# Performance work log

Hardware: AMD Instinct MI355X
Metric: run time of the kernel (lower is better)

The kernel has to match this reference:

```python
import jax, jax.numpy as jnp
import numpy as np

B, S, W = 32, 256, 32
T = 16               # topics per doc, each spanning L = S//T sentences
VOCAB, E, H, D = 400001, 300, 128, 128


def _gru_scan(x, Wih, Whh, bih, bhh, reverse=False):
    """x: [B,S,E] -> (outputs [B,S,H], final hidden [B,H]). Torch GRU cell math."""
    h0 = jnp.zeros((x.shape[0], Whh.shape[1]), x.dtype)
    gi_all = jnp.einsum('bse,ge->bsg', x, Wih) + bih  # precompute input gates [B,S,3H]

    def step(h, gi):
        gh = h @ Whh.T + bhh
        ir, iz, inn = jnp.split(gi, 3, axis=-1)
        hr, hz, hn = jnp.split(gh, 3, axis=-1)
        r = jax.nn.sigmoid(ir + hr)
        z = jax.nn.sigmoid(iz + hz)
        n = jnp.tanh(inn + r * hn)
        h_new = (1.0 - z) * n + z * h
        return h_new, h_new

    hT, hs = jax.lax.scan(step, h0, jnp.swapaxes(gi_all, 0, 1), reverse=reverse)
    return jnp.swapaxes(hs, 0, 1), hT


def setup_inputs() -> dict:
    key = jax.random.key(0)
    ks = jax.random.split(key, 16)
    sc_i = 1.0 / np.sqrt(H)
    L = S // T
    starts = (jnp.arange(T, dtype=jnp.int32) * L + 1)          # 1-based inclusive
    ends = (jnp.arange(T, dtype=jnp.int32) + 1) * L
    tse = jnp.broadcast_to(jnp.stack([starts, ends], axis=-1)[None], (B, T, 2)).astype(jnp.int32)
    return {
        'word_ids': jax.random.randint(ks[0], (B, S, W), 0, VOCAB, dtype=jnp.int32),
        'topic_start_ends': tse,
        'embed_table': jax.random.normal(ks[1], (VOCAB, E), jnp.float32) * 0.6,
        'Wih_f': jax.random.normal(ks[2], (3 * H, E), jnp.float32) * sc_i,
        'Whh_f': jax.random.normal(ks[3], (3 * H, H), jnp.float32) * sc_i,
        'bih_f': jax.random.normal(ks[4], (3 * H,), jnp.float32) * sc_i,
        'bhh_f': jax.random.normal(ks[5], (3 * H,), jnp.float32) * sc_i,
        'Wih_b': jax.random.normal(ks[6], (3 * H, E), jnp.float32) * sc_i,
        'Whh_b': jax.random.normal(ks[7], (3 * H, H), jnp.float32) * sc_i,
        'bih_b': jax.random.normal(ks[8], (3 * H,), jnp.float32) * sc_i,
        'bhh_b': jax.random.normal(ks[9], (3 * H,), jnp.float32) * sc_i,
        'v_attention': jax.random.normal(ks[10], (4 * H, 1), jnp.float32),
        'W_attention': jax.random.normal(ks[11], (4 * H, 4 * H), jnp.float32) * (1.0 / np.sqrt(4 * H)),
        'W1': jax.random.normal(ks[12], (D, 4 * H), jnp.float32) * (1.0 / np.sqrt(4 * H)),
        'b1': jax.random.normal(ks[13], (D,), jnp.float32) * 0.01,
        'W2': jax.random.normal(ks[14], (1, D), jnp.float32) * (1.0 / np.sqrt(D)),
        'b2': jax.random.normal(ks[15], (1,), jnp.float32) * 0.01,
    }


def reference(word_ids, topic_start_ends, embed_table,
              Wih_f, Whh_f, bih_f, bhh_f, Wih_b, Whh_b, bih_b, bhh_b,
              v_attention, W_attention, W1, b1, W2, b2):
    b, s, _ = word_ids.shape
    h = Whh_f.shape[1]
    # --- sent_encoder: gather word embeddings, mean-pool per sentence ---
    sent_emb = jnp.mean(embed_table[word_ids], axis=2)          # [B,S,E]
    # --- doc_encoder: bi-GRU ---
    out_f, hT_f = _gru_scan(sent_emb, Wih_f, Whh_f, bih_f, bhh_f, reverse=False)
    out_b, hT_b = _gru_scan(sent_emb, Wih_b, Whh_b, bih_b, bhh_b, reverse=True)
    sent_rep = jnp.concatenate([out_f, out_b], axis=-1)         # [B,S,2H]
    # faithful to hidden.view(batch_size, 2H) on hidden of shape [2,B,H]
    doc_vec = jnp.stack([hT_f, hT_b], axis=0).reshape(b, 2 * h)
    doc_rep = jnp.broadcast_to(doc_vec[:, None, :], (b, s, 2 * h))
    # topic reps via segment difference of cumulative GRU states (pad trick)
    pad = jnp.pad(sent_rep, ((0, 0), (1, 1), (0, 0)))           # [B,S+2,2H]
    starts = topic_start_ends[:, :, 0]                          # [B,T], 1-based
    ends = topic_start_ends[:, :, 1]

    def gat(idx, lo, hi):
        return jnp.take_along_axis(pad[..., lo:hi], idx[:, :, None], axis=1)
    fwd_part = gat(ends, 0, h) - gat(starts - 1, 0, h)
    bwd_part = gat(starts, h, 2 * h) - gat(ends + 1, h, 2 * h)
    topic_mat = jnp.concatenate([fwd_part, bwd_part], axis=-1)  # [B,T,2H]
    # scatter topic vectors to sentences: topic id = #starts at or before sentence
    sidx = jnp.arange(s, dtype=starts.dtype)
    topic_id = jnp.sum(sidx[None, :, None] >= (starts - 1)[:, None, :], axis=-1) - 1  # [B,S]
    topic_rep = jnp.take_along_axis(topic_mat, topic_id[:, :, None], axis=1)          # [B,S,2H]
    # --- decoder ---
    cat_ds = jnp.concatenate([doc_rep, sent_rep], axis=-1)      # [B,S,4H]
    cat_ts = jnp.concatenate([topic_rep, sent_rep], axis=-1)
    doc_scores = jnp.tanh(cat_ds @ W_attention) @ v_attention   # [B,S,1]
    topic_scores = jnp.tanh(cat_ts @ W_attention) @ v_attention
    doc_w = jax.nn.softmax(doc_scores, axis=1)
    topic_w = jax.nn.softmax(topic_scores, axis=1)
    context = doc_w * doc_rep + topic_w * topic_rep             # [B,S,2H]
    inp = jnp.concatenate([sent_rep, context], axis=-1)         # [B,S,4H]
    hdd = jax.nn.relu(inp @ W1.T + b1)                          # dropout = identity (eval)
    logits = (hdd @ W2.T + b2).squeeze(-1)                      # [B,S]
    return logits
```

## Files before the change

### kernel.cpp

```cpp
#include <hip/hip_runtime.h>
#include <hip/hip_bf16.h>
#include <cstdint>

#define Bk 32
#define Sk 256
#define Wk 32
#define Tk 16
#define Ek 300
#define Hk 128
#define Dk 128
#define NROWS (Bk*Sk)
#define GI_N  (3*Hk*2)

__device__ __forceinline__ float fast_sigmoid(float x) {
    return 1.f / (1.f + __expf(-x));
}
__device__ __forceinline__ float fast_tanh(float x) {
    float ax = fabsf(x);
    float e = __expf(2.f * ax);
    float t = 1.f - 2.f / (1.f + e);
    return copysignf(t, x);
}
__device__ __forceinline__ void barrier_lgkm() {
    asm volatile("s_waitcnt lgkmcnt(0)" ::: "memory");
    __builtin_amdgcn_s_barrier();
}

__global__ __launch_bounds__(256) void pack_kernel(
    const float* __restrict__ Wf, const float* __restrict__ Wb,
    const float* __restrict__ bf, const float* __restrict__ bb,
    const float* __restrict__ W1,
    float* __restrict__ Bgi, float* __restrict__ bias_gi, float* __restrict__ BW1)
{
    int idx = blockIdx.x * 256 + threadIdx.x;
    if (idx < 300 * 768) {
        int k = idx / 768, n = idx % 768;
        Bgi[idx] = (n < 384) ? Wf[n * 300 + k] : Wb[(n - 384) * 300 + k];
    }
    if (idx < 768) bias_gi[idx] = (idx < 384) ? bf[idx] : bb[idx - 384];
    if (idx < 512 * 128) {
        int k = idx >> 7, n = idx & 127;
        BW1[idx] = W1[n * 512 + k];
    }
}

__global__ __launch_bounds__(256) void embed_mean_kernel(
    const int* __restrict__ wids, const float* __restrict__ table,
    float* __restrict__ sent_emb)
{
    int wv = (blockIdx.x << 2) + (threadIdx.x >> 6);
    int lane = threadIdx.x & 63;
    if (wv >= NROWS) return;
    const int* idp = wids + (size_t)wv * Wk;
    float4 a0 = {0,0,0,0}, a1 = {0,0,0,0};
    #pragma unroll 4
    for (int w = 0; w < Wk; ++w) {
        int id = idp[w];
        const float4* r4 = reinterpret_cast<const float4*>(table + (size_t)id * Ek);
        float4 v0 = r4[lane];
        a0.x += v0.x; a0.y += v0.y; a0.z += v0.z; a0.w += v0.w;
        if (lane < 11) {
            float4 v1 = r4[64 + lane];
            a1.x += v1.x; a1.y += v1.y; a1.z += v1.z; a1.w += v1.w;
        }
    }
    const float sc = 1.f / 32.f;
    float4* o4 = reinterpret_cast<float4*>(sent_emb + (size_t)wv * Ek);
    float4 o0 = {a0.x*sc, a0.y*sc, a0.z*sc, a0.w*sc};
    o4[lane] = o0;
    if (lane < 11) {
        float4 o1 = {a1.x*sc, a1.y*sc, a1.z*sc, a1.w*sc};
        o4[64 + lane] = o1;
    }
}

template<bool BIAS, bool RELU>
__global__ __launch_bounds__(256) void gemm_kernel(
    const float* __restrict__ A, const float* __restrict__ B,
    const float* __restrict__ bias, float* __restrict__ C,
    int M, int N, int K)
{
    __shared__ float As[64][68];
    __shared__ float Bs[64][68];
    const int tid = threadIdx.x;
    const int m0 = blockIdx.x * 64;
    const int n0 = blockIdx.y * 64;
    const int tx = tid & 15, ty = tid >> 4;
    const int lr = tid >> 2;
    const int lc = tid & 3;
    float acc[4][4] = {};

    for (int k0 = 0; k0 < K; k0 += 64) {
        #pragma unroll
        for (int i = 0; i < 4; ++i) {
            int kk = lc * 4 + i * 16;
            int gm = m0 + lr;
            int gk = k0 + kk;
            float4 v = {0,0,0,0};
            if (gm < M && gk < K)
                v = *reinterpret_cast<const float4*>(A + (size_t)gm * K + gk);
            As[kk+0][lr] = v.x; As[kk+1][lr] = v.y; As[kk+2][lr] = v.z; As[kk+3][lr] = v.w;
        }
        #pragma unroll
        for (int i = 0; i < 4; ++i) {
            int nn = lc * 4 + i * 16;
            int gk = k0 + lr;
            float4 v = {0,0,0,0};
            if (gk < K)
                v = *reinterpret_cast<const float4*>(B + (size_t)gk * N + n0 + nn);
            *reinterpret_cast<float4*>(&Bs[lr][nn]) = v;
        }
        __syncthreads();
        #pragma unroll 8
        for (int k = 0; k < 64; ++k) {
            float4 av = *reinterpret_cast<const float4*>(&As[k][ty*4]);
            float4 bv = *reinterpret_cast<const float4*>(&Bs[k][tx*4]);
            acc[0][0] += av.x*bv.x; acc[0][1] += av.x*bv.y; acc[0][2] += av.x*bv.z; acc[0][3] += av.x*bv.w;
            acc[1][0] += av.y*bv.x; acc[1][1] += av.y*bv.y; acc[1][2] += av.y*bv.z; acc[1][3] += av.y*bv.w;
            acc[2][0] += av.z*bv.x; acc[2][1] += av.z*bv.y; acc[2][2] += av.z*bv.z; acc[2][3] += av.z*bv.w;
            acc[3][0] += av.w*bv.x; acc[3][1] += av.w*bv.y; acc[3][2] += av.w*bv.z; acc[3][3] += av.w*bv.w;
        }
        __syncthreads();
    }
    #pragma unroll
    for (int r = 0; r < 4; ++r) {
        int row = m0 + ty * 4 + r;
        if (row < M) {
            float4 v = {acc[r][0], acc[r][1], acc[r][2], acc[r][3]};
            if (BIAS) {
                const float* bp = bias + n0 + tx * 4;
                v.x += bp[0]; v.y += bp[1]; v.z += bp[2]; v.w += bp[3];
            }
            if (RELU) {
                v.x = fmaxf(v.x, 0.f); v.y = fmaxf(v.y, 0.f);
                v.z = fmaxf(v.z, 0.f); v.w = fmaxf(v.w, 0.f);
            }
            *reinterpret_cast<float4*>(C + (size_t)row * N + n0 + tx * 4) = v;
        }
    }
}

__global__ __launch_bounds__(768, 1) void gru_scan_kernel(
    const float* __restrict__ gi,
    const float* __restrict__ Whh_f, const float* __restrict__ Whh_b,
    const float* __restrict__ bhh_f, const float* __restrict__ bhh_b,
    float* __restrict__ sent_rep,
    float* __restrict__ hT)
{
    const int blk = blockIdx.x;
    const int dir = blk >> 5;
    const int b   = blk & 31;
    const int t = threadIdx.x;
    const int row  = t >> 1;
    const int half = t & 1;
    const float* Whh = dir ? Whh_b : Whh_f;
    const float* bhh = dir ? bhh_b : bhh_f;
    __shared__ float hsh[136];
    __shared__ float ghb[384];

    const float4* wp4 = reinterpret_cast<const float4*>(Whh + row * 128 + half * 64);
    float4 w0  = wp4[0],  w1  = wp4[1],  w2  = wp4[2],  w3  = wp4[3];
    float4 w4  = wp4[4],  w5  = wp4[5],  w6  = wp4[6],  w7  = wp4[7];
    float4 w8  = wp4[8],  w9  = wp4[9],  w10 = wp4[10], w11 = wp4[11];
    float4 w12 = wp4[12], w13 = wp4[13], w14 = wp4[14], w15 = wp4[15];
    const float bias = bhh[row];

    if (t < 136) hsh[t] = 0.f;

    float gir = 0.f, giz = 0.f, gin_ = 0.f;
    if (t < 128) {
        const int s0 = dir ? (Sk - 1) : 0;
        const float* g0 = gi + (size_t)(b * Sk + s0) * GI_N + dir * 384 + t;
        gir = g0[0]; giz = g0[128]; gin_ = g0[256];
    }
    __syncthreads();

    const float* hb = &hsh[half * 72];
    for (int step = 0; step < Sk; ++step) {
        const int s = dir ? (Sk - 1 - step) : step;
        float a0 = 0.f, a1 = 0.f, a2 = 0.f, a3 = 0.f;
        float a4 = 0.f, a5 = 0.f, a6 = 0.f, a7 = 0.f;
        #define MAC4(q, wq, aa, ab) { float4 h4 = *reinterpret_cast<const float4*>(hb + 4*(q)); \
            aa = fmaf(wq.x, h4.x, aa); ab = fmaf(wq.y, h4.y, ab); \
            aa = fmaf(wq.z, h4.z, aa); ab = fmaf(wq.w, h4.w, ab); }
        MAC4(0,w0,a0,a1)   MAC4(1,w1,a2,a3)   MAC4(2,w2,a4,a5)   MAC4(3,w3,a6,a7)
        MAC4(4,w4,a0,a1)   MAC4(5,w5,a2,a3)   MAC4(6,w6,a4,a5)   MAC4(7,w7,a6,a7)
        MAC4(8,w8,a0,a1)   MAC4(9,w9,a2,a3)   MAC4(10,w10,a4,a5) MAC4(11,w11,a6,a7)
        MAC4(12,w12,a0,a1) MAC4(13,w13,a2,a3) MAC4(14,w14,a4,a5) MAC4(15,w15,a6,a7)
        #undef MAC4
        float part = ((a0 + a1) + (a2 + a3)) + ((a4 + a5) + (a6 + a7));
        part += __shfl_xor(part, 1);
        if (half == 0) ghb[row] = part + bias;
        barrier_lgkm();
        if (t < 128) {
            const int j = t;
            float hr = ghb[j], hz = ghb[128 + j], hn = ghb[256 + j];
            float r = fast_sigmoid(gir + hr);
            float z = fast_sigmoid(giz + hz);
            float n = fast_tanh(gin_ + r * hn);
            const int ji = j + ((j >> 6) << 3);
            float hold = hsh[ji];
            float hnew = (1.f - z) * n + z * hold;
            hsh[ji] = hnew;
            sent_rep[(size_t)(b * Sk + s) * 256 + dir * 128 + j] = hnew;
            if (step < Sk - 1) {
                const int sn = dir ? (s - 1) : (s + 1);
                const float* g = gi + (size_t)(b * Sk + sn) * GI_N + dir * 384 + j;
                gir = g[0]; giz = g[128]; gin_ = g[256];
            }
        }
        barrier_lgkm();
    }
    if (t < 128) {
        const int ji = t + ((t >> 6) << 3);
        hT[dir * 4096 + b * 128 + t] = hsh[ji];
    }
}

__device__ __forceinline__ float4 sr_load_guard(const float* sr, int b, int sidx, int j4) {
    if (sidx < 0 || sidx >= Sk) { float4 z = {0,0,0,0}; return z; }
    return reinterpret_cast<const float4*>(sr)[(size_t)(b * Sk + sidx) * 64 + j4];
}
__global__ __launch_bounds__(64) void prep_kernel(
    const int* __restrict__ tse, const float* __restrict__ sent_rep,
    const float* __restrict__ hT, float* __restrict__ dvtm)
{
    const int b = blockIdx.x;
    const int t = blockIdx.y;
    const int j4 = threadIdx.x;
    if (t == 16) {
        int dir = b >> 4;
        int bb = 2 * (b & 15) + (j4 >> 5);
        int jj4 = j4 & 31;
        float4 v = reinterpret_cast<const float4*>(hT)[dir * 1024 + bb * 32 + jj4];
        reinterpret_cast<float4*>(dvtm)[b * 64 + j4] = v;
    } else {
        int st = tse[b * 32 + t * 2];
        int en = tse[b * 32 + t * 2 + 1];
        float4 va, vb;
        if (j4 < 32) {
            va = sr_load_guard(sent_rep, b, en - 1, j4);
            vb = sr_load_guard(sent_rep, b, st - 2, j4);
        } else {
            va = sr_load_guard(sent_rep, b, st - 1, j4);
            vb = sr_load_guard(sent_rep, b, en, j4);
        }
        float4 v = {va.x - vb.x, va.y - vb.y, va.z - vb.z, va.w - vb.w};
        reinterpret_cast<float4*>(dvtm)[(32 + b * 16 + t) * 64 + j4] = v;
    }
}

__global__ __launch_bounds__(256) void scores_kernel(
    const float* __restrict__ SW,
    const float* __restrict__ dptp,
    const float* __restrict__ vatt,
    const int* __restrict__ tse,
    float* __restrict__ dsc, float* __restrict__ tsc)
{
    int row = (blockIdx.x << 2) + (threadIdx.x >> 6);
    int lane = threadIdx.x & 63;
    if (row >= NROWS) return;
    int b = row >> 8, s = row & 255;
    int ti = 0;
    #pragma unroll
    for (int t = 1; t < 16; ++t) ti += (s >= tse[b * 32 + t * 2] - 1) ? 1 : 0;
    const float4* swr = reinterpret_cast<const float4*>(SW + (size_t)row * 512);
    const float4* dpr = reinterpret_cast<const float4*>(dptp + (size_t)b * 512);
    const float4* tpr = reinterpret_cast<const float4*>(dptp + (size_t)(32 + b * 16 + ti) * 512);
    const float4* vv  = reinterpret_cast<const float4*>(vatt);
    float sd = 0.f, st = 0.f;
    #pragma unroll
    for (int q = 0; q < 2; ++q) {
        int i = lane * 2 + q;
        float4 sw = swr[i], dp = dpr[i], tp = tpr[i], v = vv[i];
        sd += fast_tanh(sw.x + dp.x) * v.x + fast_tanh(sw.y + dp.y) * v.y
            + fast_tanh(sw.z + dp.z) * v.z + fast_tanh(sw.w + dp.w) * v.w;
        st += fast_tanh(sw.x + tp.x) * v.x + fast_tanh(sw.y + tp.y) * v.y
            + fast_tanh(sw.z + tp.z) * v.z + fast_tanh(sw.w + tp.w) * v.w;
    }
    #pragma unroll
    for (int off = 32; off; off >>= 1) {
        sd += __shfl_xor(sd, off);
        st += __shfl_xor(st, off);
    }
    if (lane == 0) { dsc[row] = sd; tsc[row] = st; }
}

__global__ __launch_bounds__(256) void softmax_kernel(float* __restrict__ dsc, float* __restrict__ tsc)
{
    const int b = blockIdx.x, sidx = threadIdx.x;
    const int lane = sidx & 63, wid = sidx >> 6;
    __shared__ float rd[4], rt[4];
    float d = dsc[b * Sk + sidx];
    float t = tsc[b * Sk + sidx];
    float md = d, mt = t;
    #pragma unroll
    for (int off = 32; off; off >>= 1) {
        md = fmaxf(md, __shfl_xor(md, off));
        mt = fmaxf(mt, __shfl_xor(mt, off));
    }
    if (lane == 0) { rd[wid] = md; rt[wid] = mt; }
    __syncthreads();
    md = fmaxf(fmaxf(rd[0], rd[1]), fmaxf(rd[2], rd[3]));
    mt = fmaxf(fmaxf(rt[0], rt[1]), fmaxf(rt[2], rt[3]));
    float ed = __expf(d - md), et = __expf(t - mt);
    float sd = ed, stt = et;
    #pragma unroll
    for (int off = 32; off; off >>= 1) {
        sd += __shfl_xor(sd, off);
        stt += __shfl_xor(stt, off);
    }
    __syncthreads();
    if (lane == 0) { rd[wid] = sd; rt[wid] = stt; }
    __syncthreads();
    sd = rd[0] + rd[1] + rd[2] + rd[3];
    stt = rt[0] + rt[1] + rt[2] + rt[3];
    dsc[b * Sk + sidx] = ed / sd;
    tsc[b * Sk + sidx] = et / stt;
}

__global__ __launch_bounds__(128) void build_inp_kernel(
    const float* __restrict__ sent_rep, const float* __restrict__ dvtm,
    const float* __restrict__ dw, const float* __restrict__ tw,
    const int* __restrict__ tse, float* __restrict__ inp)
{
    int row = blockIdx.x;
    int b = row >> 8, s = row & 255;
    int f4c = threadIdx.x;
    float4 v;
    if (f4c < 64) {
        v = reinterpret_cast<const float4*>(sent_rep)[(size_t)row * 64 + f4c];
    } else {
        int ti = 0;
        #pragma unroll
        for (int t = 1; t < 16; ++t) ti += (s >= tse[b * 32 + t * 2] - 1) ? 1 : 0;
        float dwv = dw[row], twv = tw[row];
        int j4 = f4c - 64;
        float4 dv = reinterpret_cast<const float4*>(dvtm)[b * 64 + j4];
        float4 tm = reinterpret_cast<const float4*>(dvtm)[(32 + b * 16 + ti) * 64 + j4];
        v.x = dwv * dv.x + twv * tm.x;
        v.y = dwv * dv.y + twv * tm.y;
        v.z = dwv * dv.z + twv * tm.z;
        v.w = dwv * dv.w + twv * tm.w;
    }
    reinterpret_cast<float4*>(inp)[(size_t)row * 128 + f4c] = v;
}

__global__ __launch_bounds__(256) void logits_kernel(
    const float* __restrict__ hdd, const float* __restrict__ W2,
    const float* __restrict__ b2, float* __restrict__ out)
{
    int row = (blockIdx.x << 2) + (threadIdx.x >> 6);
    int lane = threadIdx.x & 63;
    if (row >= NROWS) return;
    float acc = hdd[(size_t)row * 128 + lane] * W2[lane]
              + hdd[(size_t)row * 128 + 64 + lane] * W2[64 + lane];
    #pragma unroll
    for (int off = 32; off; off >>= 1) acc += __shfl_xor(acc, off);
    if (lane == 0) out[row] = acc + b2[0];
}

extern "C" void kernel_launch(void* const* d_in, const int* in_sizes, int n_in,
                              void* d_out, int out_size, void* d_ws, size_t ws_size,
                              hipStream_t stream)
{
    const int*   wids  = (const int*)d_in[0];
    const int*   tse   = (const int*)d_in[1];
    const float* table = (const float*)d_in[2];
    const float* Wihf  = (const float*)d_in[3];
    const float* Whhf  = (const float*)d_in[4];
    const float* bihf  = (const float*)d_in[5];
    const float* bhhf  = (const float*)d_in[6];
    const float* Wihb  = (const float*)d_in[7];
    const float* Whhb  = (const float*)d_in[8];
    const float* bihb  = (const float*)d_in[9];
    const float* bhhb  = (const float*)d_in[10];
    const float* vatt  = (const float*)d_in[11];
    const float* Watt  = (const float*)d_in[12];
    const float* W1    = (const float*)d_in[13];
    const float* b1    = (const float*)d_in[14];
    const float* W2    = (const float*)d_in[15];
    const float* b2    = (const float*)d_in[16];
    float* ws = (float*)d_ws;
    float* out = (float*)d_out;

    float* sent_emb = ws + 0;
    float* gi       = ws + 2457600;
    float* sent_rep = ws + 8749056;
    float* hT       = ws + 10846208;
    float* dvtm     = ws + 10854400;
    float* dptp     = ws + 10993664;
    float* dsc      = ws + 11272192;
    float* tsc      = ws + 11280384;
    float* Bgi      = ws + 11288576;
    float* bias_gi  = ws + 11518976;
    float* BW1      = ws + 11519744;
    float* SW       = ws + 0;
    float* inp      = ws + 4194304;
    float* hdd      = ws + 0;

    if (ws_size < (size_t)11585280 * sizeof(float)) return;

    pack_kernel<<<900, 256, 0, stream>>>(Wihf, Wihb, bihf, bihb, W1, Bgi, bias_gi, BW1);
    embed_mean_kernel<<<2048, 256, 0, stream>>>(wids, table, sent_emb);
    gemm_kernel<true,false><<<dim3(128, 12), 256, 0, stream>>>(sent_emb, Bgi, bias_gi, gi, NROWS, 768, 300);
    gru_scan_kernel<<<64, 768, 0, stream>>>(gi, Whhf, Whhb, bhhf, bhhb, sent_rep, hT);
    prep_kernel<<<dim3(32, 17), 64, 0, stream>>>(tse, sent_rep, hT, dvtm);
    gemm_kernel<false,false><<<dim3(128, 8), 256, 0, stream>>>(sent_rep, Watt + 256 * 512, nullptr, SW, NROWS, 512, 256);
    gemm_kernel<false,false><<<dim3(9, 8), 256, 0, stream>>>(dvtm, Watt, nullptr, dptp, 544, 512, 256);
    scores_kernel<<<2048, 256, 0, stream>>>(SW, dptp, vatt, tse, dsc, tsc);
    softmax_kernel<<<32, 256, 0, stream>>>(dsc, tsc);
    build_inp_kernel<<<NROWS, 128, 0, stream>>>(sent_rep, dvtm, dsc, tsc, tse, inp);
    gemm_kernel<true,true><<<dim3(128, 2), 256, 0, stream>>>(inp, BW1, b1, hdd, NROWS, 128, 512);
    logits_kernel<<<2048, 256, 0, stream>>>(hdd, W2, b2, out);
}
```

Measured before the change: 411.7 us.

## Remap GRU recurrent matvec so each thread computes three gate rows over a quarter of K

The recurrent matvec in the GRU scan is reorganised. Each thread now holds weights for three consecutive gate rows over a 32-element slice of the hidden state, so every hidden-state float4 read from LDS feeds three rows instead of one. Partial sums are reduced across the four K-slices with two wave shuffles, and the block shrinks from 768 to 512 threads, with the hidden-state padding changed to fit. The aim is less LDS traffic and fewer threads per barrier step, at the cost of more weight registers per thread and longer dependent FMA chains: three accumulators of length 32 instead of eight of length 8.

```diff
diff --git a/kernel.cpp b/kernel.cpp
--- a/kernel.cpp
+++ b/kernel.cpp
@@ -140,7 +140,7 @@
     }
 }
 
-__global__ __launch_bounds__(768, 1) void gru_scan_kernel(
+__global__ __launch_bounds__(512, 1) void gru_scan_kernel(
     const float* __restrict__ gi,
     const float* __restrict__ Whh_f, const float* __restrict__ Whh_b,
     const float* __restrict__ bhh_f, const float* __restrict__ bhh_b,
@@ -151,21 +151,46 @@
     const int dir = blk >> 5;
     const int b   = blk & 31;
     const int t = threadIdx.x;
-    const int row  = t >> 1;
-    const int half = t & 1;
+    const int lane = t & 63;
+    const int w_id = t >> 6;
+    const int q = lane >> 4;
+    const int m = lane & 15;
+    const int g = w_id * 16 + m;
     const float* Whh = dir ? Whh_b : Whh_f;
     const float* bhh = dir ? bhh_b : bhh_f;
-    __shared__ float hsh[136];
+    __shared__ float hsh[144];
     __shared__ float ghb[384];
 
-    const float4* wp4 = reinterpret_cast<const float4*>(Whh + row * 128 + half * 64);
-    float4 w0  = wp4[0],  w1  = wp4[1],  w2  = wp4[2],  w3  = wp4[3];
-    float4 w4  = wp4[4],  w5  = wp4[5],  w6  = wp4[6],  w7  = wp4[7];
-    float4 w8  = wp4[8],  w9  = wp4[9],  w10 = wp4[10], w11 = wp4[11];
-    float4 w12 = wp4[12], w13 = wp4[13], w14 = wp4[14], w15 = wp4[15];
-    const float bias = bhh[row];
-
-    if (t < 136) hsh[t] = 0.f;
+    const float* wr = Whh + (3 * g) * 128 + 32 * q;
+    float4 wA0 = *reinterpret_cast<const float4*>(wr +   0);
+    float4 wA1 = *reinterpret_cast<const float4*>(wr +   4);
+    float4 wA2 = *reinterpret_cast<const float4*>(wr +   8);
+    float4 wA3 = *reinterpret_cast<const float4*>(wr +  12);
+    float4 wA4 = *reinterpret_cast<const float4*>(wr +  16);
+    float4 wA5 = *reinterpret_cast<const float4*>(wr +  20);
+    float4 wA6 = *reinterpret_cast<const float4*>(wr +  24);
+    float4 wA7 = *reinterpret_cast<const float4*>(wr +  28);
+    float4 wB0 = *reinterpret_cast<const float4*>(wr + 128);
+    float4 wB1 = *reinterpret_cast<const float4*>(wr + 132);
+    float4 wB2 = *reinterpret_cast<const float4*>(wr + 136);
+    float4 wB3 = *reinterpret_cast<const float4*>(wr + 140);
+    float4 wB4 = *reinterpret_cast<const float4*>(wr + 144);
+    float4 wB5 = *reinterpret_cast<const float4*>(wr + 148);
+    float4 wB6 = *reinterpret_cast<const float4*>(wr + 152);
+    float4 wB7 = *reinterpret_cast<const float4*>(wr + 156);
+    float4 wC0 = *reinterpret_cast<const float4*>(wr + 256);
+    float4 wC1 = *reinterpret_cast<const float4*>(wr + 260);
+    float4 wC2 = *reinterpret_cast<const float4*>(wr + 264);
+    float4 wC3 = *reinterpret_cast<const float4*>(wr + 268);
+    float4 wC4 = *reinterpret_cast<const float4*>(wr + 272);
+    float4 wC5 = *reinterpret_cast<const float4*>(wr + 276);
+    float4 wC6 = *reinterpret_cast<const float4*>(wr + 280);
+    float4 wC7 = *reinterpret_cast<const float4*>(wr + 284);
+    const float b0 = bhh[3 * g + 0];
+    const float b1 = bhh[3 * g + 1];
+    const float b2 = bhh[3 * g + 2];
+
+    if (t < 144) hsh[t] = 0.f;
 
     float gir = 0.f, giz = 0.f, gin_ = 0.f;
     if (t < 128) {
@@ -175,22 +200,27 @@
     }
     __syncthreads();
 
-    const float* hb = &hsh[half * 72];
+    const float4* hseg = reinterpret_cast<const float4*>(hsh) + 9 * q;
     for (int step = 0; step < Sk; ++step) {
         const int s = dir ? (Sk - 1 - step) : step;
-        float a0 = 0.f, a1 = 0.f, a2 = 0.f, a3 = 0.f;
-        float a4 = 0.f, a5 = 0.f, a6 = 0.f, a7 = 0.f;
-        #define MAC4(q, wq, aa, ab) { float4 h4 = *reinterpret_cast<const float4*>(hb + 4*(q)); \
-            aa = fmaf(wq.x, h4.x, aa); ab = fmaf(wq.y, h4.y, ab); \
-            aa = fmaf(wq.z, h4.z, aa); ab = fmaf(wq.w, h4.w, ab); }
-        MAC4(0,w0,a0,a1)   MAC4(1,w1,a2,a3)   MAC4(2,w2,a4,a5)   MAC4(3,w3,a6,a7)
-        MAC4(4,w4,a0,a1)   MAC4(5,w5,a2,a3)   MAC4(6,w6,a4,a5)   MAC4(7,w7,a6,a7)
-        MAC4(8,w8,a0,a1)   MAC4(9,w9,a2,a3)   MAC4(10,w10,a4,a5) MAC4(11,w11,a6,a7)
-        MAC4(12,w12,a0,a1) MAC4(13,w13,a2,a3) MAC4(14,w14,a4,a5) MAC4(15,w15,a6,a7)
-        #undef MAC4
-        float part = ((a0 + a1) + (a2 + a3)) + ((a4 + a5) + (a6 + a7));
-        part += __shfl_xor(part, 1);
-        if (half == 0) ghb[row] = part + bias;
+        float pA = 0.f, pB = 0.f, pC = 0.f;
+        #define SEG(j) { float4 h4 = hseg[j]; \
+            pA = fmaf(wA##j.x, h4.x, pA); pA = fmaf(wA##j.y, h4.y, pA); \
+            pA = fmaf(wA##j.z, h4.z, pA); pA = fmaf(wA##j.w, h4.w, pA); \
+            pB = fmaf(wB##j.x, h4.x, pB); pB = fmaf(wB##j.y, h4.y, pB); \
+            pB = fmaf(wB##j.z, h4.z, pB); pB = fmaf(wB##j.w, h4.w, pB); \
+            pC = fmaf(wC##j.x, h4.x, pC); pC = fmaf(wC##j.y, h4.y, pC); \
+            pC = fmaf(wC##j.z, h4.z, pC); pC = fmaf(wC##j.w, h4.w, pC); }
+        SEG(0) SEG(1) SEG(2) SEG(3) SEG(4) SEG(5) SEG(6) SEG(7)
+        #undef SEG
+        pA += __shfl_xor(pA, 16); pA += __shfl_xor(pA, 32);
+        pB += __shfl_xor(pB, 16); pB += __shfl_xor(pB, 32);
+        pC += __shfl_xor(pC, 16); pC += __shfl_xor(pC, 32);
+        if (q == 0) {
+            ghb[3 * g + 0] = pA + b0;
+            ghb[3 * g + 1] = pB + b1;
+            ghb[3 * g + 2] = pC + b2;
+        }
         barrier_lgkm();
         if (t < 128) {
             const int j = t;
@@ -198,21 +228,21 @@
             float r = fast_sigmoid(gir + hr);
             float z = fast_sigmoid(giz + hz);
             float n = fast_tanh(gin_ + r * hn);
-            const int ji = j + ((j >> 6) << 3);
+            const int ji = 36 * (j >> 5) + (j & 31);
             float hold = hsh[ji];
             float hnew = (1.f - z) * n + z * hold;
             hsh[ji] = hnew;
             sent_rep[(size_t)(b * Sk + s) * 256 + dir * 128 + j] = hnew;
             if (step < Sk - 1) {
                 const int sn = dir ? (s - 1) : (s + 1);
-                const float* g = gi + (size_t)(b * Sk + sn) * GI_N + dir * 384 + j;
-                gir = g[0]; giz = g[128]; gin_ = g[256];
+                const float* gp = gi + (size_t)(b * Sk + sn) * GI_N + dir * 384 + j;
+                gir = gp[0]; giz = gp[128]; gin_ = gp[256];
             }
         }
         barrier_lgkm();
     }
     if (t < 128) {
-        const int ji = t + ((t >> 6) << 3);
+        const int ji = 36 * (t >> 5) + (t & 31);
         hT[dir * 4096 + b * 128 + t] = hsh[ji];
     }
 }
@@ -404,7 +434,7 @@
     pack_kernel<<<900, 256, 0, stream>>>(Wihf, Wihb, bihf, bihb, W1, Bgi, bias_gi, BW1);
     embed_mean_kernel<<<2048, 256, 0, stream>>>(wids, table, sent_emb);
     gemm_kernel<true,false><<<dim3(128, 12), 256, 0, stream>>>(sent_emb, Bgi, bias_gi, gi, NROWS, 768, 300);
-    gru_scan_kernel<<<64, 768, 0, stream>>>(gi, Whhf, Whhb, bhhf, bhhb, sent_rep, hT);
+    gru_scan_kernel<<<64, 512, 0, stream>>>(gi, Whhf, Whhb, bhhf, bhhb, sent_rep, hT);
     prep_kernel<<<dim3(32, 17), 64, 0, stream>>>(tse, sent_rep, hT, dvtm);
     gemm_kernel<false,false><<<dim3(128, 8), 256, 0, stream>>>(sent_rep, Watt + 256 * 512, nullptr, SW, NROWS, 512, 256);
     gemm_kernel<false,false><<<dim3(9, 8), 256, 0, stream>>>(dvtm, Watt, nullptr, dptp, 544, 512, 256);
```

Result: no change. 415.5 us (+0.9%).
